# Kernel tuning notes

Hardware: AMD Instinct MI355X
Metric: run time of the kernel (lower is better)

## Reference

```python
import jax, jax.numpy as jnp
import numpy as np

N_EMBD = 1024
N_HEAD = 16
HEAD_DIM = N_EMBD // N_HEAD
NEG = -1e10


def setup_inputs() -> dict:
    key = jax.random.key(0)
    ks = jax.random.split(key, 5)
    B, T, C = 4, 2048, N_EMBD
    s = 0.02
    return {
        "x": jax.random.normal(ks[0], (B, T, C), dtype=jnp.float32),
        "w_attn": jax.random.normal(ks[1], (C, 3 * C), dtype=jnp.float32) * s,
        "b_attn": jnp.zeros((3 * C,), dtype=jnp.float32),
        "w_proj": jax.random.normal(ks[2], (C, C), dtype=jnp.float32) * s,
        "b_proj": jnp.zeros((C,), dtype=jnp.float32),
    }


def reference(x, w_attn, b_attn, w_proj, b_proj):
    B, T, C = x.shape
    H, D = N_HEAD, HEAD_DIM
    qkv = x @ w_attn + b_attn                      # [B,T,3C]
    q, k, v = jnp.split(qkv, 3, axis=-1)
    q = q.reshape(B, T, H, D).transpose(0, 2, 1, 3)  # [B,H,T,D]
    k = k.reshape(B, T, H, D).transpose(0, 2, 1, 3)
    v = v.reshape(B, T, H, D).transpose(0, 2, 1, 3)
    att = jnp.einsum("bhqd,bhkd->bhqk", q, k) / jnp.sqrt(jnp.float32(D))
    # additive causal mask: strictly-upper triangle gets -1e10 (as in torch source)
    mask = jnp.triu(jnp.full((T, T), NEG, dtype=att.dtype), k=1)
    att = jax.nn.softmax(att + mask, axis=-1)
    y = jnp.einsum("bhqk,bhkd->bhqd", att, v)      # [B,H,T,D]
    y = y.transpose(0, 2, 1, 3).reshape(B, T, C)
    return y @ w_proj + b_proj
```

## Files before the change

kernel.cpp:

```cpp
#include <hip/hip_runtime.h>
#include <hip/hip_bf16.h>

#define T_SEQ 2048
#define NE    1024
#define NH    16
#define HD    64
#define QKV_N 3072
#define MROWS 8192

typedef __attribute__((ext_vector_type(8))) short short8;
typedef __attribute__((ext_vector_type(4))) float f32x4;

__device__ __forceinline__ short f2bf(float f) {
  __hip_bfloat16 h = __float2bfloat16(f);
  return *reinterpret_cast<short*>(&h);
}

__device__ __forceinline__ void lds16(const void* g, void* l) {
  __builtin_amdgcn_global_load_lds(
      (const __attribute__((address_space(1))) unsigned int*)g,
      (__attribute__((address_space(3))) unsigned int*)l, 16, 0, 0);
}

__global__ __launch_bounds__(256) void cvt_bf16(const float* __restrict__ src,
                                                short* __restrict__ dst, int n8) {
  int i = blockIdx.x * 256 + threadIdx.x;
  const int stride = gridDim.x * 256;
  for (; i < n8; i += stride) {
    const float4* s = (const float4*)(src + (size_t)i * 8);
    float4 a = s[0], b = s[1];
    short8 v = short8{f2bf(a.x), f2bf(a.y), f2bf(a.z), f2bf(a.w),
                      f2bf(b.x), f2bf(b.y), f2bf(b.z), f2bf(b.w)};
    *(short8*)(dst + (size_t)i * 8) = v;
  }
}

__global__ __launch_bounds__(256) void transpose_cvt(const float* __restrict__ src,
                                                     short* __restrict__ dst,
                                                     int K, int N) {
  __shared__ short tile[32][33];
  int bn = blockIdx.x * 32;
  int bk = blockIdx.y * 32;
  int tx = threadIdx.x;
  int ty = threadIdx.y;
#pragma unroll
  for (int i = 0; i < 32; i += 8)
    tile[ty + i][tx] = f2bf(src[(size_t)(bk + ty + i) * N + bn + tx]);
  __syncthreads();
#pragma unroll
  for (int i = 0; i < 32; i += 8)
    dst[(size_t)(bn + ty + i) * K + bk + tx] = tile[tx][ty + i];
}

__global__ __launch_bounds__(256) void transpose_v(const short* __restrict__ qkv,
                                                   short* __restrict__ vt) {
  __shared__ short tile[32][40];
  const int tt = blockIdx.x * 32;
  const int bh = blockIdx.y;
  const int dd = blockIdx.z * 32;
  const int b = bh >> 4, h = bh & 15;
  const short* src = qkv + (size_t)b * T_SEQ * QKV_N + 2 * NE + h * HD;
  int tx = threadIdx.x;
  int ty = threadIdx.y;
#pragma unroll
  for (int i = 0; i < 32; i += 8)
    tile[ty + i][tx] = src[(size_t)(tt + ty + i) * QKV_N + dd + tx];
  __syncthreads();
  short* dst = vt + (size_t)bh * HD * T_SEQ;
#pragma unroll
  for (int i = 0; i < 32; i += 8)
    dst[(size_t)(dd + ty + i) * T_SEQ + tt + tx] = tile[tx][ty + i];
}

template <bool OUTF32>
__global__ __launch_bounds__(256) void gemm_bt_bias(const short* __restrict__ A,
                                                    const short* __restrict__ Bt,
                                                    const float* __restrict__ bias,
                                                    void* __restrict__ Co,
                                                    int M, int N, int K) {
  __shared__ __align__(16) short As[128 * 32];
  __shared__ __align__(16) short Bs[128 * 32];

  const int m0 = blockIdx.x * 128;
  const int n0 = blockIdx.y * 128;
  const int tid = threadIdx.x;
  const int w = tid >> 6, lane = tid & 63;
  const int L15 = lane & 15, quad = lane >> 4;
  const int wr = (w >> 1) * 64, wc = (w & 1) * 64;

  f32x4 acc[4][4] = {};

  for (int k0 = 0; k0 < K; k0 += 32) {
    __syncthreads();

#pragma unroll
    for (int p = 0; p < 2; ++p) {
      int r = p * 64 + w * 16 + (lane >> 2);
      int gl = (lane & 3) ^ ((r >> 1) & 3);
      lds16(A + (size_t)(m0 + r) * K + k0 + gl * 8, (char*)As + p * 4096 + w * 1024);
      lds16(Bt + (size_t)(n0 + r) * K + k0 + gl * 8, (char*)Bs + p * 4096 + w * 1024);
    }

    __syncthreads();

    short8 af[4], bfr[4];
#pragma unroll
    for (int i = 0; i < 4; ++i) {
      int r = wr + i * 16 + L15;
      af[i] = *(const short8*)(As + r * 32 + (quad ^ ((r >> 1) & 3)) * 8);
    }
#pragma unroll
    for (int j = 0; j < 4; ++j) {
      int r = wc + j * 16 + L15;
      bfr[j] = *(const short8*)(Bs + r * 32 + (quad ^ ((r >> 1) & 3)) * 8);
    }
#pragma unroll
    for (int i = 0; i < 4; ++i)
#pragma unroll
      for (int j = 0; j < 4; ++j)
        acc[i][j] = __builtin_amdgcn_mfma_f32_16x16x32_bf16(af[i], bfr[j], acc[i][j], 0, 0, 0);
  }

  float bv[4];
#pragma unroll
  for (int j = 0; j < 4; ++j) bv[j] = bias[n0 + wc + j * 16 + L15];
#pragma unroll
  for (int i = 0; i < 4; ++i)
#pragma unroll
    for (int j = 0; j < 4; ++j)
#pragma unroll
      for (int r = 0; r < 4; ++r) {
        size_t row = (size_t)(m0 + wr + i * 16 + quad * 4 + r);
        int col = n0 + wc + j * 16 + L15;
        float v = acc[i][j][r] + bv[j];
        if (OUTF32)
          ((float*)Co)[row * N + col] = v;
        else
          ((short*)Co)[row * N + col] = f2bf(v);
      }
}

__global__ __launch_bounds__(256) void attn_flash(const short* __restrict__ qkv,
                                                  const short* __restrict__ vt,
                                                  short* __restrict__ y) {
  const int bx = blockIdx.x;
  const int bh = blockIdx.y;
  const int b = bh >> 4, h = bh & 15;
  const short* base = qkv + (size_t)b * T_SEQ * QKV_N;
  const int tid = threadIdx.x;
  const int w = tid >> 6, lane = tid & 63;
  const int L15 = lane & 15, quad = lane >> 4;

  __shared__ __align__(16) short Ks[2][64 * 64];
  __shared__ __align__(16) short Vs[2][64 * 64];
  __shared__ __align__(16) short Ps[4][32 * 72];

  const short one = (short)0x3F80;
  const short8 vone = short8{one, one, one, one, one, one, one, one};

  const float cs = 0.18033688011112042f;

  const short* kb_ = base + NE + h * HD;
  const short* vb_ = vt + (size_t)bh * HD * T_SEQ;

  const int srow = lane >> 3;
  const int sg = lane & 7;

  int cur = 0;

#pragma unroll 1
  for (int seg = 0; seg < 2; ++seg) {
    const int qt = seg == 0 ? (T_SEQ / 128 - 1 - bx) : bx;

    short8 qf[2][2];
#pragma unroll
    for (int qs = 0; qs < 2; ++qs) {
      const short* qp =
          base + (size_t)(qt * 128 + w * 32 + qs * 16 + L15) * QKV_N + h * HD + quad * 8;
      qf[qs][0] = *(const short8*)qp;
      qf[qs][1] = *(const short8*)(qp + 32);
    }

    f32x4 O[2][4] = {};
    f32x4 L[2] = {};

    const int nkt = 2 * qt + 2;

#pragma unroll
    for (int p = 0; p < 2; ++p) {
      int r = p * 32 + w * 8 + srow;
      int gl = sg ^ (r & 7);
      lds16(kb_ + (size_t)r * QKV_N + gl * 8, (char*)&Ks[cur][0] + p * 4096 + w * 1024);
      lds16(vb_ + (size_t)r * T_SEQ + gl * 8, (char*)&Vs[cur][0] + p * 4096 + w * 1024);
    }
    __syncthreads();

    for (int kt = 0; kt < nkt; ++kt) {
      if (kt + 1 < nkt) {
#pragma unroll
        for (int p = 0; p < 2; ++p) {
          int r = p * 32 + w * 8 + srow;
          int gl = sg ^ (r & 7);
          lds16(kb_ + (size_t)((kt + 1) * 64 + r) * QKV_N + gl * 8,
                (char*)&Ks[cur ^ 1][0] + p * 4096 + w * 1024);
          lds16(vb_ + (size_t)r * T_SEQ + (kt + 1) * 64 + gl * 8,
                (char*)&Vs[cur ^ 1][0] + p * 4096 + w * 1024);
        }
      }
      const short* K_ = &Ks[cur][0];
      const short* V_ = &Vs[cur][0];

      f32x4 S[2][4] = {};
#pragma unroll
      for (int nb = 0; nb < 4; ++nb) {
        int r = nb * 16 + L15;
        short8 kb0 = *(const short8*)&K_[r * 64 + ((quad ^ (r & 7)) * 8)];
        short8 kb1 = *(const short8*)&K_[r * 64 + (((quad + 4) ^ (r & 7)) * 8)];
#pragma unroll
        for (int qs = 0; qs < 2; ++qs) {
          S[qs][nb] = __builtin_amdgcn_mfma_f32_16x16x32_bf16(qf[qs][0], kb0, S[qs][nb], 0, 0, 0);
          S[qs][nb] = __builtin_amdgcn_mfma_f32_16x16x32_bf16(qf[qs][1], kb1, S[qs][nb], 0, 0, 0);
        }
      }

      if (kt >= nkt - 2) {
#pragma unroll
        for (int qs = 0; qs < 2; ++qs)
#pragma unroll
          for (int nb = 0; nb < 4; ++nb) {
            int kg = kt * 64 + nb * 16 + L15;
#pragma unroll
            for (int r = 0; r < 4; ++r) {
              int qg = qt * 128 + w * 32 + qs * 16 + quad * 4 + r;
              if (kg > qg) S[qs][nb][r] = -1e30f;
            }
          }
      }

      short* myP = &Ps[w][0];
#pragma unroll
      for (int qs = 0; qs < 2; ++qs)
#pragma unroll
        for (int nb = 0; nb < 4; ++nb)
#pragma unroll
          for (int r = 0; r < 4; ++r)
            myP[(qs * 16 + quad * 4 + r) * 72 + nb * 16 + L15] =
                f2bf(__builtin_amdgcn_exp2f(S[qs][nb][r] * cs));
      asm volatile("" ::: "memory");
      short8 pf[2][2];
#pragma unroll
      for (int qs = 0; qs < 2; ++qs) {
        pf[qs][0] = *(const short8*)&myP[(qs * 16 + L15) * 72 + quad * 8];
        pf[qs][1] = *(const short8*)&myP[(qs * 16 + L15) * 72 + 32 + quad * 8];
      }

#pragma unroll
      for (int nb = 0; nb < 4; ++nb) {
        int r = nb * 16 + L15;
        short8 vf0 = *(const short8*)&V_[r * 64 + ((quad ^ (r & 7)) * 8)];
        short8 vf1 = *(const short8*)&V_[r * 64 + (((quad + 4) ^ (r & 7)) * 8)];
#pragma unroll
        for (int qs = 0; qs < 2; ++qs) {
          O[qs][nb] = __builtin_amdgcn_mfma_f32_16x16x32_bf16(pf[qs][0], vf0, O[qs][nb], 0, 0, 0);
          O[qs][nb] = __builtin_amdgcn_mfma_f32_16x16x32_bf16(pf[qs][1], vf1, O[qs][nb], 0, 0, 0);
        }
      }
#pragma unroll
      for (int qs = 0; qs < 2; ++qs) {
        L[qs] = __builtin_amdgcn_mfma_f32_16x16x32_bf16(pf[qs][0], vone, L[qs], 0, 0, 0);
        L[qs] = __builtin_amdgcn_mfma_f32_16x16x32_bf16(pf[qs][1], vone, L[qs], 0, 0, 0);
      }

      __syncthreads();
      cur ^= 1;
    }

#pragma unroll
    for (int qs = 0; qs < 2; ++qs) {
      float inv[4];
#pragma unroll
      for (int r = 0; r < 4; ++r) inv[r] = 1.0f / L[qs][r];
#pragma unroll
      for (int nb = 0; nb < 4; ++nb)
#pragma unroll
        for (int r = 0; r < 4; ++r) {
          size_t row =
              (size_t)b * T_SEQ + (size_t)(qt * 128 + w * 32 + qs * 16 + quad * 4 + r);
          int col = h * HD + nb * 16 + L15;
          y[row * NE + col] = f2bf(O[qs][nb][r] * inv[r]);
        }
    }
  }
}

extern "C" void kernel_launch(void* const* d_in, const int* in_sizes, int n_in,
                              void* d_out, int out_size, void* d_ws, size_t ws_size,
                              hipStream_t stream) {
  (void)in_sizes; (void)n_in; (void)out_size; (void)ws_size;
  const float* x      = (const float*)d_in[0];
  const float* w_attn = (const float*)d_in[1];
  const float* b_attn = (const float*)d_in[2];
  const float* w_proj = (const float*)d_in[3];
  const float* b_proj = (const float*)d_in[4];
  float* out = (float*)d_out;

  short* qkv = (short*)d_ws;
  short* wT2 = qkv;
  short* wT1 = qkv + (size_t)MROWS * QKV_N;
  short* y   = wT1;

  short* xb = (short*)d_out;
  short* vt = (short*)d_out + (size_t)MROWS * NE;

  cvt_bf16<<<2048, 256, 0, stream>>>(x, xb, MROWS * NE / 8);

  transpose_cvt<<<dim3(QKV_N / 32, NE / 32), dim3(32, 8), 0, stream>>>(w_attn, wT1, NE, QKV_N);

  gemm_bt_bias<false><<<dim3(MROWS / 128, QKV_N / 128), 256, 0, stream>>>(
      xb, wT1, b_attn, qkv, MROWS, QKV_N, NE);

  transpose_v<<<dim3(T_SEQ / 32, 64, 2), dim3(32, 8), 0, stream>>>(qkv, vt);

  attn_flash<<<dim3(T_SEQ / 256, 64), 256, 0, stream>>>(qkv, vt, y);

  transpose_cvt<<<dim3(NE / 32, NE / 32), dim3(32, 8), 0, stream>>>(w_proj, wT2, NE, NE);

  gemm_bt_bias<true><<<dim3(MROWS / 128, NE / 128), 256, 0, stream>>>(
      y, wT2, b_proj, out, MROWS, NE, NE);
}
```

Measured before the change: 280.6 us.

## Shrink attention query tile to 64, single-buffer K/V, swizzle block order

The flash-attention kernel now gives each block two 64-row query tiles (paired for causal balance) instead of 128-row tiles, so the grid doubles to 1024 blocks. Each wave now handles 16 query rows. K/V double buffering is dropped in favour of a single LDS buffer loaded synchronously each iteration, which cuts LDS use to raise occupancy. Block indices are swizzled across heads, and s_setprio is raised around the MFMA sections. The trade-off is more K/V reloads per query row and load latency that is no longer hidden by prefetch, in exchange for more parallelism and resident blocks.

```diff
diff --git a/kernel.cpp b/kernel.cpp
--- a/kernel.cpp
+++ b/kernel.cpp
@@ -143,17 +143,19 @@
 __global__ __launch_bounds__(256) void attn_flash(const short* __restrict__ qkv,
                                                   const short* __restrict__ vt,
                                                   short* __restrict__ y) {
-  const int bx = blockIdx.x;
-  const int bh = blockIdx.y;
+  const int lid = (int)(blockIdx.x + gridDim.x * blockIdx.y);
+  const int swz = (lid & 7) * 128 + (lid >> 3);
+  const int bx = swz & 15;
+  const int bh = swz >> 4;
   const int b = bh >> 4, h = bh & 15;
   const short* base = qkv + (size_t)b * T_SEQ * QKV_N;
   const int tid = threadIdx.x;
   const int w = tid >> 6, lane = tid & 63;
   const int L15 = lane & 15, quad = lane >> 4;
 
-  __shared__ __align__(16) short Ks[2][64 * 64];
-  __shared__ __align__(16) short Vs[2][64 * 64];
-  __shared__ __align__(16) short Ps[4][32 * 72];
+  __shared__ __align__(16) short Ks[64 * 64];
+  __shared__ __align__(16) short Vs[64 * 64];
+  __shared__ __align__(16) short Ps[4][16 * 72];
 
   const short one = (short)0x3F80;
   const short8 vone = short8{one, one, one, one, one, one, one, one};
@@ -166,130 +168,94 @@
   const int srow = lane >> 3;
   const int sg = lane & 7;
 
-  int cur = 0;
-
 #pragma unroll 1
   for (int seg = 0; seg < 2; ++seg) {
-    const int qt = seg == 0 ? (T_SEQ / 128 - 1 - bx) : bx;
-
-    short8 qf[2][2];
-#pragma unroll
-    for (int qs = 0; qs < 2; ++qs) {
+    const int qt = seg == 0 ? (T_SEQ / 64 - 1 - bx) : bx;
+
+    short8 qf0, qf1;
+    {
       const short* qp =
-          base + (size_t)(qt * 128 + w * 32 + qs * 16 + L15) * QKV_N + h * HD + quad * 8;
-      qf[qs][0] = *(const short8*)qp;
-      qf[qs][1] = *(const short8*)(qp + 32);
-    }
-
-    f32x4 O[2][4] = {};
-    f32x4 L[2] = {};
-
-    const int nkt = 2 * qt + 2;
-
-#pragma unroll
-    for (int p = 0; p < 2; ++p) {
-      int r = p * 32 + w * 8 + srow;
-      int gl = sg ^ (r & 7);
-      lds16(kb_ + (size_t)r * QKV_N + gl * 8, (char*)&Ks[cur][0] + p * 4096 + w * 1024);
-      lds16(vb_ + (size_t)r * T_SEQ + gl * 8, (char*)&Vs[cur][0] + p * 4096 + w * 1024);
-    }
-    __syncthreads();
-
+          base + (size_t)(qt * 64 + w * 16 + L15) * QKV_N + h * HD + quad * 8;
+      qf0 = *(const short8*)qp;
+      qf1 = *(const short8*)(qp + 32);
+    }
+
+    f32x4 O[4] = {};
+    f32x4 Lsum = {};
+
+    const int nkt = qt + 1;
     for (int kt = 0; kt < nkt; ++kt) {
-      if (kt + 1 < nkt) {
-#pragma unroll
-        for (int p = 0; p < 2; ++p) {
-          int r = p * 32 + w * 8 + srow;
-          int gl = sg ^ (r & 7);
-          lds16(kb_ + (size_t)((kt + 1) * 64 + r) * QKV_N + gl * 8,
-                (char*)&Ks[cur ^ 1][0] + p * 4096 + w * 1024);
-          lds16(vb_ + (size_t)r * T_SEQ + (kt + 1) * 64 + gl * 8,
-                (char*)&Vs[cur ^ 1][0] + p * 4096 + w * 1024);
-        }
-      }
-      const short* K_ = &Ks[cur][0];
-      const short* V_ = &Vs[cur][0];
-
-      f32x4 S[2][4] = {};
+      __syncthreads();
+
+#pragma unroll
+      for (int p = 0; p < 2; ++p) {
+        int r = p * 32 + w * 8 + srow;
+        int gl = sg ^ (r & 7);
+        lds16(kb_ + (size_t)(kt * 64 + r) * QKV_N + gl * 8, (char*)Ks + p * 4096 + w * 1024);
+        lds16(vb_ + (size_t)r * T_SEQ + kt * 64 + gl * 8, (char*)Vs + p * 4096 + w * 1024);
+      }
+      __syncthreads();
+
+      f32x4 S[4] = {};
+      __builtin_amdgcn_s_setprio(1);
 #pragma unroll
       for (int nb = 0; nb < 4; ++nb) {
         int r = nb * 16 + L15;
-        short8 kb0 = *(const short8*)&K_[r * 64 + ((quad ^ (r & 7)) * 8)];
-        short8 kb1 = *(const short8*)&K_[r * 64 + (((quad + 4) ^ (r & 7)) * 8)];
-#pragma unroll
-        for (int qs = 0; qs < 2; ++qs) {
-          S[qs][nb] = __builtin_amdgcn_mfma_f32_16x16x32_bf16(qf[qs][0], kb0, S[qs][nb], 0, 0, 0);
-          S[qs][nb] = __builtin_amdgcn_mfma_f32_16x16x32_bf16(qf[qs][1], kb1, S[qs][nb], 0, 0, 0);
+        short8 kb0 = *(const short8*)&Ks[r * 64 + ((quad ^ (r & 7)) * 8)];
+        short8 kb1 = *(const short8*)&Ks[r * 64 + (((quad + 4) ^ (r & 7)) * 8)];
+        S[nb] = __builtin_amdgcn_mfma_f32_16x16x32_bf16(qf0, kb0, S[nb], 0, 0, 0);
+        S[nb] = __builtin_amdgcn_mfma_f32_16x16x32_bf16(qf1, kb1, S[nb], 0, 0, 0);
+      }
+      __builtin_amdgcn_s_setprio(0);
+
+      if (kt == nkt - 1) {
+#pragma unroll
+        for (int nb = 0; nb < 4; ++nb) {
+          int kg = kt * 64 + nb * 16 + L15;
+#pragma unroll
+          for (int r = 0; r < 4; ++r) {
+            int qg = qt * 64 + w * 16 + quad * 4 + r;
+            if (kg > qg) S[nb][r] = -1e30f;
+          }
         }
       }
 
-      if (kt >= nkt - 2) {
-#pragma unroll
-        for (int qs = 0; qs < 2; ++qs)
-#pragma unroll
-          for (int nb = 0; nb < 4; ++nb) {
-            int kg = kt * 64 + nb * 16 + L15;
-#pragma unroll
-            for (int r = 0; r < 4; ++r) {
-              int qg = qt * 128 + w * 32 + qs * 16 + quad * 4 + r;
-              if (kg > qg) S[qs][nb][r] = -1e30f;
-            }
-          }
-      }
-
       short* myP = &Ps[w][0];
 #pragma unroll
-      for (int qs = 0; qs < 2; ++qs)
-#pragma unroll
-        for (int nb = 0; nb < 4; ++nb)
-#pragma unroll
-          for (int r = 0; r < 4; ++r)
-            myP[(qs * 16 + quad * 4 + r) * 72 + nb * 16 + L15] =
-                f2bf(__builtin_amdgcn_exp2f(S[qs][nb][r] * cs));
+      for (int nb = 0; nb < 4; ++nb)
+#pragma unroll
+        for (int r = 0; r < 4; ++r)
+          myP[(quad * 4 + r) * 72 + nb * 16 + L15] =
+              f2bf(__builtin_amdgcn_exp2f(S[nb][r] * cs));
       asm volatile("" ::: "memory");
-      short8 pf[2][2];
-#pragma unroll
-      for (int qs = 0; qs < 2; ++qs) {
-        pf[qs][0] = *(const short8*)&myP[(qs * 16 + L15) * 72 + quad * 8];
-        pf[qs][1] = *(const short8*)&myP[(qs * 16 + L15) * 72 + 32 + quad * 8];
-      }
-
+      short8 pf0 = *(const short8*)&myP[L15 * 72 + quad * 8];
+      short8 pf1 = *(const short8*)&myP[L15 * 72 + 32 + quad * 8];
+
+      __builtin_amdgcn_s_setprio(1);
 #pragma unroll
       for (int nb = 0; nb < 4; ++nb) {
         int r = nb * 16 + L15;
-        short8 vf0 = *(const short8*)&V_[r * 64 + ((quad ^ (r & 7)) * 8)];
-        short8 vf1 = *(const short8*)&V_[r * 64 + (((quad + 4) ^ (r & 7)) * 8)];
-#pragma unroll
-        for (int qs = 0; qs < 2; ++qs) {
-          O[qs][nb] = __builtin_amdgcn_mfma_f32_16x16x32_bf16(pf[qs][0], vf0, O[qs][nb], 0, 0, 0);
-          O[qs][nb] = __builtin_amdgcn_mfma_f32_16x16x32_bf16(pf[qs][1], vf1, O[qs][nb], 0, 0, 0);
-        }
-      }
-#pragma unroll
-      for (int qs = 0; qs < 2; ++qs) {
-        L[qs] = __builtin_amdgcn_mfma_f32_16x16x32_bf16(pf[qs][0], vone, L[qs], 0, 0, 0);
-        L[qs] = __builtin_amdgcn_mfma_f32_16x16x32_bf16(pf[qs][1], vone, L[qs], 0, 0, 0);
-      }
-
-      __syncthreads();
-      cur ^= 1;
-    }
-
-#pragma unroll
-    for (int qs = 0; qs < 2; ++qs) {
-      float inv[4];
-#pragma unroll
-      for (int r = 0; r < 4; ++r) inv[r] = 1.0f / L[qs][r];
-#pragma unroll
-      for (int nb = 0; nb < 4; ++nb)
-#pragma unroll
-        for (int r = 0; r < 4; ++r) {
-          size_t row =
-              (size_t)b * T_SEQ + (size_t)(qt * 128 + w * 32 + qs * 16 + quad * 4 + r);
-          int col = h * HD + nb * 16 + L15;
-          y[row * NE + col] = f2bf(O[qs][nb][r] * inv[r]);
-        }
-    }
+        short8 vf0 = *(const short8*)&Vs[r * 64 + ((quad ^ (r & 7)) * 8)];
+        short8 vf1 = *(const short8*)&Vs[r * 64 + (((quad + 4) ^ (r & 7)) * 8)];
+        O[nb] = __builtin_amdgcn_mfma_f32_16x16x32_bf16(pf0, vf0, O[nb], 0, 0, 0);
+        O[nb] = __builtin_amdgcn_mfma_f32_16x16x32_bf16(pf1, vf1, O[nb], 0, 0, 0);
+      }
+      Lsum = __builtin_amdgcn_mfma_f32_16x16x32_bf16(pf0, vone, Lsum, 0, 0, 0);
+      Lsum = __builtin_amdgcn_mfma_f32_16x16x32_bf16(pf1, vone, Lsum, 0, 0, 0);
+      __builtin_amdgcn_s_setprio(0);
+    }
+
+    float inv[4];
+#pragma unroll
+    for (int r = 0; r < 4; ++r) inv[r] = 1.0f / Lsum[r];
+#pragma unroll
+    for (int nb = 0; nb < 4; ++nb)
+#pragma unroll
+      for (int r = 0; r < 4; ++r) {
+        size_t row = (size_t)b * T_SEQ + (size_t)(qt * 64 + w * 16 + quad * 4 + r);
+        int col = h * HD + nb * 16 + L15;
+        y[row * NE + col] = f2bf(O[nb][r] * inv[r]);
+      }
   }
 }
 
@@ -321,7 +287,7 @@
 
   transpose_v<<<dim3(T_SEQ / 32, 64, 2), dim3(32, 8), 0, stream>>>(qkv, vt);
 
-  attn_flash<<<dim3(T_SEQ / 256, 64), 256, 0, stream>>>(qkv, vt, y);
+  attn_flash<<<dim3(16, 64), 256, 0, stream>>>(qkv, vt, y);
 
   transpose_cvt<<<dim3(NE / 32, NE / 32), dim3(32, 8), 0, stream>>>(w_proj, wT2, NE, NE);
 
```

Result: no change. 282.9 us (+0.8%).
